# Kernel tuning notes

Hardware: AMD Instinct MI355X
Metric: run time of the kernel (lower is better)

Reference implementation:

```python
import jax, jax.numpy as jnp
import numpy as np

N_NODES = 50000
N_EDGES = 600000
N_FEAT = 128
N_GRAPHS = 256
DIM = 95
N_OUT = 12
N_ITER = 10
BN_EPS = 1e-5


def setup_inputs() -> dict:
    key = jax.random.key(0)
    ks = jax.random.split(key, 16)
    inp = {}
    inp["x"] = jax.random.normal(ks[0], (N_NODES, N_FEAT), dtype=jnp.float32)
    inp["edge_index"] = jax.random.randint(ks[1], (2, N_EDGES), 0, N_NODES, dtype=jnp.int64)
    inp["batch"] = jnp.sort(jax.random.randint(ks[2], (N_NODES,), 0, N_GRAPHS, dtype=jnp.int64))
    def lin(k, fan_in, fan_out):
        bound = 1.0 / np.sqrt(fan_in)
        kw, kb = jax.random.split(k)
        W = jax.random.uniform(kw, (fan_in, fan_out), jnp.float32, -bound, bound)
        b = jax.random.uniform(kb, (fan_out,), jnp.float32, -bound, bound)
        return W, b
    inp["W1a"], inp["b1a"] = lin(ks[3], N_FEAT, N_FEAT)            # nn1 layer 1
    inp["W1b"], inp["b1b"] = lin(ks[4], N_FEAT, N_FEAT)            # nn1 layer 2
    inp["gamma"] = jnp.ones((N_FEAT,), jnp.float32)                 # bn1 weight
    inp["beta"] = jnp.zeros((N_FEAT,), jnp.float32)                 # bn1 bias
    inp["Wl1"], inp["bl1"] = lin(ks[5], 2 * N_FEAT, N_FEAT // 2)   # lin1
    inp["Wl2"], inp["bl2"] = lin(ks[6], 2 * N_FEAT, N_FEAT // 2)   # lin2
    inp["Wm1"], inp["bm1"] = lin(ks[7], N_FEAT, DIM)               # MLP layer 1
    inp["Wm2"], inp["bm2"] = lin(ks[8], DIM, N_OUT)                # MLP layer 2
    return inp


def reference(x, edge_index, batch, W1a, b1a, W1b, b1b, gamma, beta,
              Wl1, bl1, Wl2, bl2, Wm1, bm1, Wm2, bm2):
    src, dst = edge_index[0], edge_index[1]
    # GINConv (eps=0): h_i = nn1(x_i + sum_{j->i} x_j)
    agg = jax.ops.segment_sum(x[src], dst, num_segments=N_NODES)
    h0 = x + agg
    h0 = jax.nn.relu(h0 @ W1a + b1a) @ W1b + b1b
    x1 = jax.nn.relu(h0)
    # BatchNorm1d (training mode: batch statistics, biased variance)
    mean = jnp.mean(x1, axis=0)
    var = jnp.mean(jnp.square(x1 - mean), axis=0)
    x1 = gamma * (x1 - mean) * jax.lax.rsqrt(var + BN_EPS) + beta
    # global_mean_pool over graph ids
    sums = jax.ops.segment_sum(x1, batch, num_segments=N_GRAPHS)
    counts = jax.ops.segment_sum(jnp.ones((N_NODES,), x1.dtype), batch, num_segments=N_GRAPHS)
    xg = sums / jnp.maximum(counts, 1.0)[:, None]
    # recurrent gated loop
    h = xg
    for _ in range(N_ITER):
        cat = jnp.concatenate([xg, h], axis=1)          # [G, 2*F]
        p = cat @ Wl1 + bl1
        q = cat @ Wl2 + bl2
        h = jnp.concatenate([jnp.tanh(q), jax.nn.sigmoid(p)], axis=1)
    # output MLP
    return jax.nn.relu(h @ Wm1 + bm1) @ Wm2 + bm2
```

## Files before the change

kernel.cpp:

```cpp
#include <hip/hip_runtime.h>
#include <cstddef>

#define N_NODES  50000
#define N_EDGES  600000
#define N_FEAT   128
#define N_GRAPHS 256
#define DIMM     95
#define N_OUTD   12
#define N_ITERS  10

#define N_CHUNKS 196

#define WS_BUF   0
#define WS_STATS (N_NODES * N_FEAT)
#define WS_SCALE (WS_STATS + 256)
#define WS_XG    (WS_SCALE + 256)
#define WS_CNT   (WS_XG + N_GRAPHS * N_FEAT)
#define WS_OFF   (WS_CNT + N_NODES)
#define WS_CUR   (WS_OFF + N_NODES + 4)
#define WS_CHS   (WS_CUR + N_NODES)
#define WS_SORT  (WS_CHS + 256)

#define SR 132

__global__ void k_zero(float* __restrict__ ws) {
    int i = blockIdx.x * 256 + threadIdx.x;
    int* cnt = (int*)ws + WS_CNT;
    if (i < N_NODES) cnt[i] = 0;
    if (blockIdx.x == 0) ws[WS_STATS + threadIdx.x] = 0.f;
}

__global__ void k_hist(const int* __restrict__ ei, float* __restrict__ ws) {
    int e = blockIdx.x * 256 + threadIdx.x;
    int* cnt = (int*)ws + WS_CNT;
    if (e < N_EDGES) atomicAdd(&cnt[ei[N_EDGES + e]], 1);
}

__global__ void k_chunk(float* __restrict__ ws) {
    __shared__ int red[4];
    const int tid = threadIdx.x;
    int* cnt = (int*)ws + WS_CNT;
    int i = blockIdx.x * 256 + tid;
    int v = (i < N_NODES) ? cnt[i] : 0;
    #pragma unroll
    for (int d = 32; d; d >>= 1) v += __shfl_down(v, d);
    if ((tid & 63) == 0) red[tid >> 6] = v;
    __syncthreads();
    if (tid == 0) ((int*)ws + WS_CHS)[blockIdx.x] = red[0] + red[1] + red[2] + red[3];
}

__global__ void k_scan0(float* __restrict__ ws) {
    __shared__ int s[256];
    const int tid = threadIdx.x;
    int* chs = (int*)ws + WS_CHS;
    int v = (tid < N_CHUNKS) ? chs[tid] : 0;
    s[tid] = v;
    __syncthreads();
    #pragma unroll
    for (int d = 1; d < 256; d <<= 1) {
        int t = (tid >= d) ? s[tid - d] : 0;
        __syncthreads();
        s[tid] += t;
        __syncthreads();
    }
    if (tid < N_CHUNKS) chs[tid] = s[tid] - v;
    if (tid == 0) ((int*)ws + WS_OFF)[N_NODES] = N_EDGES;
}

__global__ void k_scan1(float* __restrict__ ws) {
    __shared__ int s[256];
    const int tid = threadIdx.x;
    int* cnt = (int*)ws + WS_CNT;
    int* off = (int*)ws + WS_OFF;
    int* cur = (int*)ws + WS_CUR;
    int i = blockIdx.x * 256 + tid;
    int v = (i < N_NODES) ? cnt[i] : 0;
    s[tid] = v;
    __syncthreads();
    #pragma unroll
    for (int d = 1; d < 256; d <<= 1) {
        int t = (tid >= d) ? s[tid - d] : 0;
        __syncthreads();
        s[tid] += t;
        __syncthreads();
    }
    int o = ((int*)ws + WS_CHS)[blockIdx.x] + s[tid] - v;
    if (i < N_NODES) { off[i] = o; cur[i] = o; }
}

__global__ void k_scatter(const int* __restrict__ ei, float* __restrict__ ws) {
    int e = blockIdx.x * 256 + threadIdx.x;
    if (e >= N_EDGES) return;
    int d = ei[N_EDGES + e];
    int s = ei[e];
    int* cur = (int*)ws + WS_CUR;
    int pos = atomicAdd(&cur[d], 1);
    ((int*)ws + WS_SORT)[pos] = s;
}

__global__ __launch_bounds__(256) void k_gather(const float* __restrict__ x,
                                                float* __restrict__ ws) {
    const int tid  = threadIdx.x;
    const int lane = tid & 63;
    const int wv   = tid >> 6;
    const int r = blockIdx.x * 4 + wv;
    if (r >= N_NODES) return;
    const int* off = (const int*)ws + WS_OFF;
    const int* ss  = (const int*)ws + WS_SORT;
    const int lo = off[r], hi = off[r + 1];
    float acc0 = x[(size_t)r * N_FEAT + lane];
    float acc1 = x[(size_t)r * N_FEAT + 64 + lane];
    int e = lo;
    for (; e + 4 <= hi; e += 4) {
        int s0 = ss[e], s1 = ss[e + 1], s2 = ss[e + 2], s3 = ss[e + 3];
        const float* p0 = x + (size_t)s0 * N_FEAT;
        const float* p1 = x + (size_t)s1 * N_FEAT;
        const float* p2 = x + (size_t)s2 * N_FEAT;
        const float* p3 = x + (size_t)s3 * N_FEAT;
        float a0 = p0[lane], b0 = p0[64 + lane];
        float a1 = p1[lane], b1 = p1[64 + lane];
        float a2 = p2[lane], b2 = p2[64 + lane];
        float a3 = p3[lane], b3 = p3[64 + lane];
        acc0 += a0 + a1 + a2 + a3;
        acc1 += b0 + b1 + b2 + b3;
    }
    for (; e < hi; ++e) {
        const float* p = x + (size_t)ss[e] * N_FEAT;
        acc0 += p[lane];
        acc1 += p[64 + lane];
    }
    float* buf = ws + WS_BUF;
    buf[(size_t)r * N_FEAT + lane]      = acc0;
    buf[(size_t)r * N_FEAT + 64 + lane] = acc1;
}

__global__ __launch_bounds__(256, 2) void k_mlp(float* __restrict__ buf,
        const float* __restrict__ W1a, const float* __restrict__ b1a,
        const float* __restrict__ W1b, const float* __restrict__ b1b) {
    __shared__ float As[64 * SR];
    __shared__ float Ts[64 * SR];
    const int tid = threadIdx.x;
    const int fg = tid & 15;
    const int rg = tid >> 4;
    const int row0 = blockIdx.x * 64;

    #pragma unroll
    for (int p = 0; p < 8; ++p) {
        int f4 = tid + p * 256;
        int r = f4 >> 5, c = (f4 & 31) * 4;
        float4 v = make_float4(0.f, 0.f, 0.f, 0.f);
        if (row0 + r < N_NODES) v = *(const float4*)(buf + (size_t)(row0 + r) * N_FEAT + c);
        *(float4*)(As + r * SR + c) = v;
    }
    __syncthreads();

    float acc[4][8];
    #pragma unroll
    for (int i = 0; i < 4; ++i)
        #pragma unroll
        for (int j = 0; j < 8; ++j) acc[i][j] = 0.f;

    #pragma unroll 4
    for (int k = 0; k < N_FEAT; ++k) {
        const float4 w0 = *(const float4*)(W1a + k * N_FEAT + fg * 8);
        const float4 w1 = *(const float4*)(W1a + k * N_FEAT + fg * 8 + 4);
        #pragma unroll
        for (int i = 0; i < 4; ++i) {
            const float a = As[(rg * 4 + i) * SR + k];
            acc[i][0] += a * w0.x; acc[i][1] += a * w0.y;
            acc[i][2] += a * w0.z; acc[i][3] += a * w0.w;
            acc[i][4] += a * w1.x; acc[i][5] += a * w1.y;
            acc[i][6] += a * w1.z; acc[i][7] += a * w1.w;
        }
    }
    {
        const float4 ba0 = *(const float4*)(b1a + fg * 8);
        const float4 ba1 = *(const float4*)(b1a + fg * 8 + 4);
        #pragma unroll
        for (int i = 0; i < 4; ++i) {
            float4 u0, u1;
            u0.x = fmaxf(acc[i][0] + ba0.x, 0.f); u0.y = fmaxf(acc[i][1] + ba0.y, 0.f);
            u0.z = fmaxf(acc[i][2] + ba0.z, 0.f); u0.w = fmaxf(acc[i][3] + ba0.w, 0.f);
            u1.x = fmaxf(acc[i][4] + ba1.x, 0.f); u1.y = fmaxf(acc[i][5] + ba1.y, 0.f);
            u1.z = fmaxf(acc[i][6] + ba1.z, 0.f); u1.w = fmaxf(acc[i][7] + ba1.w, 0.f);
            *(float4*)(Ts + (rg * 4 + i) * SR + fg * 8)     = u0;
            *(float4*)(Ts + (rg * 4 + i) * SR + fg * 8 + 4) = u1;
        }
    }
    __syncthreads();

    #pragma unroll
    for (int i = 0; i < 4; ++i)
        #pragma unroll
        for (int j = 0; j < 8; ++j) acc[i][j] = 0.f;

    #pragma unroll 4
    for (int k = 0; k < N_FEAT; ++k) {
        const float4 w0 = *(const float4*)(W1b + k * N_FEAT + fg * 8);
        const float4 w1 = *(const float4*)(W1b + k * N_FEAT + fg * 8 + 4);
        #pragma unroll
        for (int i = 0; i < 4; ++i) {
            const float a = Ts[(rg * 4 + i) * SR + k];
            acc[i][0] += a * w0.x; acc[i][1] += a * w0.y;
            acc[i][2] += a * w0.z; acc[i][3] += a * w0.w;
            acc[i][4] += a * w1.x; acc[i][5] += a * w1.y;
            acc[i][6] += a * w1.z; acc[i][7] += a * w1.w;
        }
    }
    {
        const float4 bb0 = *(const float4*)(b1b + fg * 8);
        const float4 bb1 = *(const float4*)(b1b + fg * 8 + 4);
        #pragma unroll
        for (int i = 0; i < 4; ++i) {
            int r = row0 + rg * 4 + i;
            if (r < N_NODES) {
                float4 u0, u1;
                u0.x = fmaxf(acc[i][0] + bb0.x, 0.f); u0.y = fmaxf(acc[i][1] + bb0.y, 0.f);
                u0.z = fmaxf(acc[i][2] + bb0.z, 0.f); u0.w = fmaxf(acc[i][3] + bb0.w, 0.f);
                u1.x = fmaxf(acc[i][4] + bb1.x, 0.f); u1.y = fmaxf(acc[i][5] + bb1.y, 0.f);
                u1.z = fmaxf(acc[i][6] + bb1.z, 0.f); u1.w = fmaxf(acc[i][7] + bb1.w, 0.f);
                *(float4*)(buf + (size_t)r * N_FEAT + fg * 8)     = u0;
                *(float4*)(buf + (size_t)r * N_FEAT + fg * 8 + 4) = u1;
            }
        }
    }
}

__global__ void k_stats(const float* __restrict__ buf, float* __restrict__ stats) {
    __shared__ float S[8][128];
    __shared__ float Q[8][128];
    const int tid = threadIdx.x;
    const int cg = tid & 31;
    const int rg = tid >> 5;
    float4 s = make_float4(0.f, 0.f, 0.f, 0.f);
    float4 q = make_float4(0.f, 0.f, 0.f, 0.f);
    for (int r = blockIdx.x * 8 + rg; r < N_NODES; r += gridDim.x * 8) {
        float4 v = *(const float4*)(buf + (size_t)r * N_FEAT + cg * 4);
        s.x += v.x; s.y += v.y; s.z += v.z; s.w += v.w;
        q.x += v.x * v.x; q.y += v.y * v.y; q.z += v.z * v.z; q.w += v.w * v.w;
    }
    S[rg][cg * 4 + 0] = s.x; S[rg][cg * 4 + 1] = s.y;
    S[rg][cg * 4 + 2] = s.z; S[rg][cg * 4 + 3] = s.w;
    Q[rg][cg * 4 + 0] = q.x; Q[rg][cg * 4 + 1] = q.y;
    Q[rg][cg * 4 + 2] = q.z; Q[rg][cg * 4 + 3] = q.w;
    __syncthreads();
    if (tid < 128) {
        float t = 0.f;
        #pragma unroll
        for (int g = 0; g < 8; ++g) t += S[g][tid];
        unsafeAtomicAdd(stats + tid, t);
    } else {
        int c = tid - 128;
        float t = 0.f;
        #pragma unroll
        for (int g = 0; g < 8; ++g) t += Q[g][c];
        unsafeAtomicAdd(stats + 128 + c, t);
    }
}

__global__ void k_finalize(const float* __restrict__ gamma, const float* __restrict__ beta,
                           float* __restrict__ ws) {
    int c = threadIdx.x;
    float mean = ws[WS_STATS + c] * (1.f / N_NODES);
    float var  = fmaxf(ws[WS_STATS + 128 + c] * (1.f / N_NODES) - mean * mean, 0.f);
    float sc = gamma[c] * rsqrtf(var + 1e-5f);
    ws[WS_SCALE + c] = sc;
    ws[WS_SCALE + 128 + c] = beta[c] - mean * sc;
}

__device__ __forceinline__ int lbound(const int* __restrict__ a, int n, int v) {
    int lo = 0, hi = n;
    while (lo < hi) { int m = (lo + hi) >> 1; if (a[m] < v) lo = m + 1; else hi = m; }
    return lo;
}

__global__ void k_pool(const float* __restrict__ buf, const int* __restrict__ batch,
                       float* __restrict__ ws) {
    __shared__ float S[8][128];
    __shared__ int range[2];
    const int g = blockIdx.x, tid = threadIdx.x;
    if (tid == 0) {
        range[0] = lbound(batch, N_NODES, g);
        range[1] = lbound(batch, N_NODES, g + 1);
    }
    __syncthreads();
    const int lo = range[0], hi = range[1];
    const int cg = tid & 31, rg = tid >> 5;
    float4 s = make_float4(0.f, 0.f, 0.f, 0.f);
    for (int r = lo + rg; r < hi; r += 8) {
        float4 v = *(const float4*)(buf + (size_t)r * N_FEAT + cg * 4);
        s.x += v.x; s.y += v.y; s.z += v.z; s.w += v.w;
    }
    S[rg][cg * 4 + 0] = s.x; S[rg][cg * 4 + 1] = s.y;
    S[rg][cg * 4 + 2] = s.z; S[rg][cg * 4 + 3] = s.w;
    __syncthreads();
    if (tid < 128) {
        float t = 0.f;
        #pragma unroll
        for (int g8 = 0; g8 < 8; ++g8) t += S[g8][tid];
        int cnt = hi - lo;
        float sc = ws[WS_SCALE + tid], sh = ws[WS_SCALE + 128 + tid];
        ws[WS_XG + g * N_FEAT + tid] = (cnt > 0) ? (sc * t / (float)cnt + sh) : 0.f;
    }
}

__global__ __launch_bounds__(256) void k_recur(const float* __restrict__ ws,
        const float* __restrict__ Wl1, const float* __restrict__ bl1,
        const float* __restrict__ Wl2, const float* __restrict__ bl2,
        const float* __restrict__ Wm1, const float* __restrict__ bm1,
        const float* __restrict__ Wm2, const float* __restrict__ bm2,
        float* __restrict__ out) {
    __shared__ float W1h[128 * 64];
    __shared__ float W2h[128 * 64];
    __shared__ float xg_s[128];
    __shared__ float h_s[128];
    __shared__ float px[2][64];
    __shared__ float pq[2][2][64];
    __shared__ float m_s[DIMM];
    const int g = blockIdx.x, tid = threadIdx.x;

    for (int i = tid; i < 128 * 64; i += 256) {
        W1h[i] = Wl1[128 * 64 + i];
        W2h[i] = Wl2[128 * 64 + i];
    }
    if (tid < 128) {
        float v = ws[WS_XG + g * N_FEAT + tid];
        xg_s[tid] = v;
        h_s[tid] = v;
    }
    __syncthreads();

    const int sel  = tid >> 7;
    const int part = (tid >> 6) & 1;
    const int j    = tid & 63;

    {
        const float* Wg = sel ? Wl2 : Wl1;
        float a = 0.f;
        const int k0 = part * 64;
        #pragma unroll 4
        for (int k = 0; k < 64; ++k) a += xg_s[k0 + k] * Wg[(k0 + k) * 64 + j];
        pq[sel][part][j] = a;
    }
    __syncthreads();
    if (part == 0) {
        const float* bias = sel ? bl2 : bl1;
        px[sel][j] = pq[sel][0][j] + pq[sel][1][j] + bias[j];
    }
    __syncthreads();

    const float* Wh = sel ? W2h : W1h;
    for (int it = 0; it < N_ITERS; ++it) {
        float a = 0.f;
        const int k0 = part * 64;
        #pragma unroll
        for (int k = 0; k < 64; k += 4) {
            const float4 h4 = *(const float4*)(h_s + k0 + k);
            a += h4.x * Wh[(k0 + k + 0) * 64 + j];
            a += h4.y * Wh[(k0 + k + 1) * 64 + j];
            a += h4.z * Wh[(k0 + k + 2) * 64 + j];
            a += h4.w * Wh[(k0 + k + 3) * 64 + j];
        }
        pq[sel][part][j] = a;
        __syncthreads();
        if (part == 0) {
            float tot = pq[sel][0][j] + pq[sel][1][j] + px[sel][j];
            if (sel == 0) h_s[64 + j] = 1.f / (1.f + expf(-tot));
            else          h_s[j] = tanhf(tot);
        }
        __syncthreads();
    }

    if (tid < DIMM) {
        float a = bm1[tid];
        #pragma unroll 4
        for (int k = 0; k < 128; ++k) a += h_s[k] * Wm1[k * DIMM + tid];
        m_s[tid] = fmaxf(a, 0.f);
    }
    __syncthreads();
    if (tid < N_OUTD) {
        float a = bm2[tid];
        for (int k = 0; k < DIMM; ++k) a += m_s[k] * Wm2[k * N_OUTD + tid];
        out[g * N_OUTD + tid] = a;
    }
}

extern "C" void kernel_launch(void* const* d_in, const int* in_sizes, int n_in,
                              void* d_out, int out_size, void* d_ws, size_t ws_size,
                              hipStream_t stream) {
    const float* x     = (const float*)d_in[0];
    const int*   ei    = (const int*)d_in[1];
    const int*   batch = (const int*)d_in[2];
    const float* W1a = (const float*)d_in[3];
    const float* b1a = (const float*)d_in[4];
    const float* W1b = (const float*)d_in[5];
    const float* b1b = (const float*)d_in[6];
    const float* gamma = (const float*)d_in[7];
    const float* beta  = (const float*)d_in[8];
    const float* Wl1 = (const float*)d_in[9];
    const float* bl1 = (const float*)d_in[10];
    const float* Wl2 = (const float*)d_in[11];
    const float* bl2 = (const float*)d_in[12];
    const float* Wm1 = (const float*)d_in[13];
    const float* bm1 = (const float*)d_in[14];
    const float* Wm2 = (const float*)d_in[15];
    const float* bm2 = (const float*)d_in[16];
    float* out = (float*)d_out;
    float* ws  = (float*)d_ws;

    k_zero   <<<(N_NODES + 255) / 256, 256, 0, stream>>>(ws);
    k_hist   <<<(N_EDGES + 255) / 256, 256, 0, stream>>>(ei, ws);
    k_chunk  <<<N_CHUNKS, 256, 0, stream>>>(ws);
    k_scan0  <<<1, 256, 0, stream>>>(ws);
    k_scan1  <<<N_CHUNKS, 256, 0, stream>>>(ws);
    k_scatter<<<(N_EDGES + 255) / 256, 256, 0, stream>>>(ei, ws);
    k_gather <<<(N_NODES + 3) / 4, 256, 0, stream>>>(x, ws);
    k_mlp    <<<(N_NODES + 63) / 64, 256, 0, stream>>>(ws + WS_BUF, W1a, b1a, W1b, b1b);
    k_stats  <<<512, 256, 0, stream>>>(ws + WS_BUF, ws + WS_STATS);
    k_finalize<<<1, 128, 0, stream>>>(gamma, beta, ws);
    k_pool   <<<N_GRAPHS, 256, 0, stream>>>(ws + WS_BUF, batch, ws);
    k_recur  <<<N_GRAPHS, 256, 0, stream>>>(ws, Wl1, bl1, Wl2, bl2, Wm1, bm1, Wm2, bm2, out);
}
```

Before: 336.3 us.

## Fuse neighbor gather into MLP kernel and vectorize shared-memory K loop

Merges the CSR gather kernel into the two-layer MLP kernel, so each 64-row block aggregates neighbor features straight into shared memory. This removes the intermediate buffer write and read plus one launch. It reuses a single shared tile for both layers, halving LDS use and raising the occupancy hint to 4. The K loop now reads float4 from shared memory and 4 weight rows at a time. The risk is that each wave handles 16 rows serially during the gather, which lowers memory-level parallelism for the irregular gather phase, and the weight registers add pressure.

```diff
diff --git a/kernel.cpp b/kernel.cpp
--- a/kernel.cpp
+++ b/kernel.cpp
@@ -98,59 +98,51 @@
     ((int*)ws + WS_SORT)[pos] = s;
 }
 
-__global__ __launch_bounds__(256) void k_gather(const float* __restrict__ x,
-                                                float* __restrict__ ws) {
+__global__ __launch_bounds__(256, 4) void k_fused(const float* __restrict__ x,
+        float* __restrict__ ws,
+        const float* __restrict__ W1a, const float* __restrict__ b1a,
+        const float* __restrict__ W1b, const float* __restrict__ b1b) {
+    __shared__ float As[64 * SR];
     const int tid  = threadIdx.x;
     const int lane = tid & 63;
     const int wv   = tid >> 6;
-    const int r = blockIdx.x * 4 + wv;
-    if (r >= N_NODES) return;
+    const int fg   = tid & 15;
+    const int rg   = tid >> 4;
+    const int row0 = blockIdx.x * 64;
+
     const int* off = (const int*)ws + WS_OFF;
     const int* ss  = (const int*)ws + WS_SORT;
-    const int lo = off[r], hi = off[r + 1];
-    float acc0 = x[(size_t)r * N_FEAT + lane];
-    float acc1 = x[(size_t)r * N_FEAT + 64 + lane];
-    int e = lo;
-    for (; e + 4 <= hi; e += 4) {
-        int s0 = ss[e], s1 = ss[e + 1], s2 = ss[e + 2], s3 = ss[e + 3];
-        const float* p0 = x + (size_t)s0 * N_FEAT;
-        const float* p1 = x + (size_t)s1 * N_FEAT;
-        const float* p2 = x + (size_t)s2 * N_FEAT;
-        const float* p3 = x + (size_t)s3 * N_FEAT;
-        float a0 = p0[lane], b0 = p0[64 + lane];
-        float a1 = p1[lane], b1 = p1[64 + lane];
-        float a2 = p2[lane], b2 = p2[64 + lane];
-        float a3 = p3[lane], b3 = p3[64 + lane];
-        acc0 += a0 + a1 + a2 + a3;
-        acc1 += b0 + b1 + b2 + b3;
-    }
-    for (; e < hi; ++e) {
-        const float* p = x + (size_t)ss[e] * N_FEAT;
-        acc0 += p[lane];
-        acc1 += p[64 + lane];
-    }
-    float* buf = ws + WS_BUF;
-    buf[(size_t)r * N_FEAT + lane]      = acc0;
-    buf[(size_t)r * N_FEAT + 64 + lane] = acc1;
-}
-
-__global__ __launch_bounds__(256, 2) void k_mlp(float* __restrict__ buf,
-        const float* __restrict__ W1a, const float* __restrict__ b1a,
-        const float* __restrict__ W1b, const float* __restrict__ b1b) {
-    __shared__ float As[64 * SR];
-    __shared__ float Ts[64 * SR];
-    const int tid = threadIdx.x;
-    const int fg = tid & 15;
-    const int rg = tid >> 4;
-    const int row0 = blockIdx.x * 64;
-
-    #pragma unroll
-    for (int p = 0; p < 8; ++p) {
-        int f4 = tid + p * 256;
-        int r = f4 >> 5, c = (f4 & 31) * 4;
-        float4 v = make_float4(0.f, 0.f, 0.f, 0.f);
-        if (row0 + r < N_NODES) v = *(const float4*)(buf + (size_t)(row0 + r) * N_FEAT + c);
-        *(float4*)(As + r * SR + c) = v;
+
+    for (int ii = 0; ii < 16; ++ii) {
+        const int i = wv * 16 + ii;
+        const int r = row0 + i;
+        float a0 = 0.f, a1 = 0.f;
+        if (r < N_NODES) {
+            a0 = x[(size_t)r * N_FEAT + lane];
+            a1 = x[(size_t)r * N_FEAT + 64 + lane];
+            const int lo = off[r], hi = off[r + 1];
+            int e = lo;
+            for (; e + 4 <= hi; e += 4) {
+                int s0 = ss[e], s1 = ss[e + 1], s2 = ss[e + 2], s3 = ss[e + 3];
+                const float* p0 = x + (size_t)s0 * N_FEAT;
+                const float* p1 = x + (size_t)s1 * N_FEAT;
+                const float* p2 = x + (size_t)s2 * N_FEAT;
+                const float* p3 = x + (size_t)s3 * N_FEAT;
+                float u0 = p0[lane], v0 = p0[64 + lane];
+                float u1 = p1[lane], v1 = p1[64 + lane];
+                float u2 = p2[lane], v2 = p2[64 + lane];
+                float u3 = p3[lane], v3 = p3[64 + lane];
+                a0 += u0 + u1 + u2 + u3;
+                a1 += v0 + v1 + v2 + v3;
+            }
+            for (; e < hi; ++e) {
+                const float* p = x + (size_t)ss[e] * N_FEAT;
+                a0 += p[lane];
+                a1 += p[64 + lane];
+            }
+        }
+        As[i * SR + lane]      = a0;
+        As[i * SR + 64 + lane] = a1;
     }
     __syncthreads();
 
@@ -160,19 +152,33 @@
         #pragma unroll
         for (int j = 0; j < 8; ++j) acc[i][j] = 0.f;
 
-    #pragma unroll 4
-    for (int k = 0; k < N_FEAT; ++k) {
-        const float4 w0 = *(const float4*)(W1a + k * N_FEAT + fg * 8);
-        const float4 w1 = *(const float4*)(W1a + k * N_FEAT + fg * 8 + 4);
+    #pragma unroll 2
+    for (int k = 0; k < N_FEAT; k += 4) {
+        float4 w[8];
+        #pragma unroll
+        for (int kk = 0; kk < 4; ++kk) {
+            w[2 * kk]     = *(const float4*)(W1a + (k + kk) * N_FEAT + fg * 8);
+            w[2 * kk + 1] = *(const float4*)(W1a + (k + kk) * N_FEAT + fg * 8 + 4);
+        }
         #pragma unroll
         for (int i = 0; i < 4; ++i) {
-            const float a = As[(rg * 4 + i) * SR + k];
-            acc[i][0] += a * w0.x; acc[i][1] += a * w0.y;
-            acc[i][2] += a * w0.z; acc[i][3] += a * w0.w;
-            acc[i][4] += a * w1.x; acc[i][5] += a * w1.y;
-            acc[i][6] += a * w1.z; acc[i][7] += a * w1.w;
-        }
-    }
+            const float4 a4 = *(const float4*)(As + (rg * 4 + i) * SR + k);
+            const float av[4] = {a4.x, a4.y, a4.z, a4.w};
+            #pragma unroll
+            for (int kk = 0; kk < 4; ++kk) {
+                acc[i][0] += av[kk] * w[2 * kk].x;
+                acc[i][1] += av[kk] * w[2 * kk].y;
+                acc[i][2] += av[kk] * w[2 * kk].z;
+                acc[i][3] += av[kk] * w[2 * kk].w;
+                acc[i][4] += av[kk] * w[2 * kk + 1].x;
+                acc[i][5] += av[kk] * w[2 * kk + 1].y;
+                acc[i][6] += av[kk] * w[2 * kk + 1].z;
+                acc[i][7] += av[kk] * w[2 * kk + 1].w;
+            }
+        }
+    }
+    __syncthreads();
+
     {
         const float4 ba0 = *(const float4*)(b1a + fg * 8);
         const float4 ba1 = *(const float4*)(b1a + fg * 8 + 4);
@@ -183,8 +189,8 @@
             u0.z = fmaxf(acc[i][2] + ba0.z, 0.f); u0.w = fmaxf(acc[i][3] + ba0.w, 0.f);
             u1.x = fmaxf(acc[i][4] + ba1.x, 0.f); u1.y = fmaxf(acc[i][5] + ba1.y, 0.f);
             u1.z = fmaxf(acc[i][6] + ba1.z, 0.f); u1.w = fmaxf(acc[i][7] + ba1.w, 0.f);
-            *(float4*)(Ts + (rg * 4 + i) * SR + fg * 8)     = u0;
-            *(float4*)(Ts + (rg * 4 + i) * SR + fg * 8 + 4) = u1;
+            *(float4*)(As + (rg * 4 + i) * SR + fg * 8)     = u0;
+            *(float4*)(As + (rg * 4 + i) * SR + fg * 8 + 4) = u1;
         }
     }
     __syncthreads();
@@ -194,20 +200,33 @@
         #pragma unroll
         for (int j = 0; j < 8; ++j) acc[i][j] = 0.f;
 
-    #pragma unroll 4
-    for (int k = 0; k < N_FEAT; ++k) {
-        const float4 w0 = *(const float4*)(W1b + k * N_FEAT + fg * 8);
-        const float4 w1 = *(const float4*)(W1b + k * N_FEAT + fg * 8 + 4);
+    #pragma unroll 2
+    for (int k = 0; k < N_FEAT; k += 4) {
+        float4 w[8];
+        #pragma unroll
+        for (int kk = 0; kk < 4; ++kk) {
+            w[2 * kk]     = *(const float4*)(W1b + (k + kk) * N_FEAT + fg * 8);
+            w[2 * kk + 1] = *(const float4*)(W1b + (k + kk) * N_FEAT + fg * 8 + 4);
+        }
         #pragma unroll
         for (int i = 0; i < 4; ++i) {
-            const float a = Ts[(rg * 4 + i) * SR + k];
-            acc[i][0] += a * w0.x; acc[i][1] += a * w0.y;
-            acc[i][2] += a * w0.z; acc[i][3] += a * w0.w;
-            acc[i][4] += a * w1.x; acc[i][5] += a * w1.y;
-            acc[i][6] += a * w1.z; acc[i][7] += a * w1.w;
+            const float4 a4 = *(const float4*)(As + (rg * 4 + i) * SR + k);
+            const float av[4] = {a4.x, a4.y, a4.z, a4.w};
+            #pragma unroll
+            for (int kk = 0; kk < 4; ++kk) {
+                acc[i][0] += av[kk] * w[2 * kk].x;
+                acc[i][1] += av[kk] * w[2 * kk].y;
+                acc[i][2] += av[kk] * w[2 * kk].z;
+                acc[i][3] += av[kk] * w[2 * kk].w;
+                acc[i][4] += av[kk] * w[2 * kk + 1].x;
+                acc[i][5] += av[kk] * w[2 * kk + 1].y;
+                acc[i][6] += av[kk] * w[2 * kk + 1].z;
+                acc[i][7] += av[kk] * w[2 * kk + 1].w;
+            }
         }
     }
     {
+        float* __restrict__ buf = ws + WS_BUF;
         const float4 bb0 = *(const float4*)(b1b + fg * 8);
         const float4 bb1 = *(const float4*)(b1b + fg * 8 + 4);
         #pragma unroll
@@ -414,8 +433,7 @@
     k_scan0  <<<1, 256, 0, stream>>>(ws);
     k_scan1  <<<N_CHUNKS, 256, 0, stream>>>(ws);
     k_scatter<<<(N_EDGES + 255) / 256, 256, 0, stream>>>(ei, ws);
-    k_gather <<<(N_NODES + 3) / 4, 256, 0, stream>>>(x, ws);
-    k_mlp    <<<(N_NODES + 63) / 64, 256, 0, stream>>>(ws + WS_BUF, W1a, b1a, W1b, b1b);
+    k_fused  <<<(N_NODES + 63) / 64, 256, 0, stream>>>(x, ws, W1a, b1a, W1b, b1b);
     k_stats  <<<512, 256, 0, stream>>>(ws + WS_BUF, ws + WS_STATS);
     k_finalize<<<1, 128, 0, stream>>>(gamma, beta, ws);
     k_pool   <<<N_GRAPHS, 256, 0, stream>>>(ws + WS_BUF, batch, ws);
```

Result: no change. 342.2 us (+1.8%).
